# Kernel tuning notes

Hardware: AMD Instinct MI355X
Metric: run time of the kernel (lower is better)

## Reference

```python
import jax, jax.numpy as jnp
import numpy as np

EPS = 1e-5


def conv2d(x, w, b, groups=1):
    # x: NCHW, w: OIHW, stride 1, SAME padding (== padding=k//2 for odd k)
    y = jax.lax.conv_general_dilated(
        x, w, window_strides=(1, 1), padding='SAME',
        dimension_numbers=('NCHW', 'OIHW', 'NCHW'),
        feature_group_count=groups)
    return y + b[None, :, None, None]


def gelu(x):
    return jax.nn.gelu(x, approximate=False)  # torch default GELU is exact erf


def adaptive_feature_norm(x, gamma, beta, s1w, s1b, s2w, s2b):
    # stats_net: GAP -> 1x1 conv -> ReLU -> 1x1 conv -> chunk into (gamma_a, beta_a)
    pooled = x.mean(axis=(2, 3), keepdims=True)                 # [B,C,1,1]
    h = jax.nn.relu(conv2d(pooled, s1w, s1b))
    stats = conv2d(h, s2w, s2b)                                 # [B,2C,1,1]
    ag, ab = jnp.split(stats, 2, axis=1)
    mean = x.mean(axis=(2, 3), keepdims=True)
    n = x.shape[2] * x.shape[3]
    var = ((x - mean) ** 2).sum(axis=(2, 3), keepdims=True) / (n - 1)  # unbiased, torch.var_mean default
    x_norm = (x - mean) * jax.lax.rsqrt(var + EPS)
    return (1 + ag) * gamma * x_norm + ab * beta


def setup_inputs() -> dict:
    key = jax.random.key(0)
    ks = jax.random.split(key, 40)
    B, C, H, W = 16, 256, 96, 96
    c4 = C // 4

    def n(k, shape, s=0.02):
        return jax.random.normal(k, shape, dtype=jnp.float32) * s

    inp = dict(
        x=jax.random.normal(ks[0], (B, C, H, W), dtype=jnp.float32),
        # branch1 conv1: dim -> dim//4, 3x3
        b1_conv1_w=n(ks[1], (c4, C, 3, 3)), b1_conv1_b=jnp.zeros((c4,), jnp.float32),
        # AFN on dim//4
        afn1_gamma=jnp.ones((1, c4, 1, 1), jnp.float32), afn1_beta=jnp.zeros((1, c4, 1, 1), jnp.float32),
        afn1_s1_w=n(ks[2], (c4 // 4, c4, 1, 1)), afn1_s1_b=jnp.zeros((c4 // 4,), jnp.float32),
        afn1_s2_w=n(ks[3], (c4 * 2, c4 // 4, 1, 1)), afn1_s2_b=jnp.zeros((c4 * 2,), jnp.float32),
        # branch1 conv2: dim//4 -> dim, 3x3
        b1_conv2_w=n(ks[4], (C, c4, 3, 3)), b1_conv2_b=jnp.zeros((C,), jnp.float32),
        # AFN on dim
        afn2_gamma=jnp.ones((1, C, 1, 1), jnp.float32), afn2_beta=jnp.zeros((1, C, 1, 1), jnp.float32),
        afn2_s1_w=n(ks[5], (c4, C, 1, 1)), afn2_s1_b=jnp.zeros((c4,), jnp.float32),
        afn2_s2_w=n(ks[6], (C * 2, c4, 1, 1)), afn2_s2_b=jnp.zeros((C * 2,), jnp.float32),
        # attention qkv/proj (1x1 convs)
        qkv_w=n(ks[7], (3 * C, C, 1, 1)), qkv_b=jnp.zeros((3 * C,), jnp.float32),
        proj_w=n(ks[8], (C, C, 1, 1)), proj_b=jnp.zeros((C,), jnp.float32),
        # 3 frequency decomposition branches, stacked
        # grouped 3x3 conv: groups=C//4, in=C (4 per group), out=C//4 (1 per group) -> weight [C//4, 4, 3, 3]
        fd_dw_w=n(ks[9], (3, c4, 4, 3, 3)), fd_dw_b=jnp.zeros((3, c4), jnp.float32),
        fd_pw_w=n(ks[10], (3, C, c4, 1, 1)), fd_pw_b=jnp.zeros((3, C), jnp.float32),
        freq_weights=jnp.ones((3,), jnp.float32),
        # router: GAP -> 1x1 conv -> softmax over 2 routes
        router_w=n(ks[11], (2, C, 1, 1)), router_b=jnp.zeros((2,), jnp.float32),
    )
    return inp


def reference(x,
              b1_conv1_w, b1_conv1_b, afn1_gamma, afn1_beta, afn1_s1_w, afn1_s1_b, afn1_s2_w, afn1_s2_b,
              b1_conv2_w, b1_conv2_b, afn2_gamma, afn2_beta, afn2_s1_w, afn2_s1_b, afn2_s2_w, afn2_s2_b,
              qkv_w, qkv_b, proj_w, proj_b, fd_dw_w, fd_dw_b, fd_pw_w, fd_pw_b, freq_weights,
              router_w, router_b):
    B, C, H, W = x.shape
    num_heads = 8
    hd = C // num_heads
    scale = C ** (-0.5)

    # ---- router ----
    pooled = x.mean(axis=(2, 3), keepdims=True)
    route = jax.nn.softmax(conv2d(pooled, router_w, router_b), axis=1)  # [B,2,1,1]

    # ---- branch1: conv -> AFN -> GELU -> conv -> AFN ----
    h = conv2d(x, b1_conv1_w, b1_conv1_b)
    h = adaptive_feature_norm(h, afn1_gamma, afn1_beta, afn1_s1_w, afn1_s1_b, afn1_s2_w, afn1_s2_b)
    h = gelu(h)
    h = conv2d(h, b1_conv2_w, b1_conv2_b)
    out1 = adaptive_feature_norm(h, afn2_gamma, afn2_beta, afn2_s1_w, afn2_s1_b, afn2_s2_w, afn2_s2_b)

    # ---- branch2: multi-scale frequency attention ----
    qkv = conv2d(x, qkv_w, qkv_b).reshape(B, 3, num_heads, hd, H, W)
    q, k, v = qkv[:, 0], qkv[:, 1], qkv[:, 2]          # [B, nh, hd, H, W]
    # attn over spatial rows: q @ k^T contracts W -> [B, nh, hd, H, H]
    attn = jnp.einsum('bndhw,bndgw->bndhg', q, k) * scale
    attn = jax.nn.softmax(attn, axis=-1)
    a = jnp.einsum('bndhg,bndgw->bndhw', attn, v)       # [B, nh, hd, H, W]
    # torch: .transpose(1, 2).reshape(B, C, H, W)  (hd-major channel order)
    a = a.transpose(0, 2, 1, 3, 4).reshape(B, C, H, W)
    x_attn = conv2d(a, proj_w, proj_b)

    fw = jax.nn.softmax(freq_weights, axis=0)
    freq_out = 0.0
    for i in range(3):
        f = conv2d(x, fd_dw_w[i], fd_dw_b[i], groups=C // 4)
        f = conv2d(gelu(f), fd_pw_w[i], fd_pw_b[i])
        freq_out = freq_out + fw[i] * f
    out2 = x_attn + freq_out

    return x + route[:, 0:1, :, :] * out1 + route[:, 1:2, :, :] * out2
```

## Files before the change

### kernel.cpp

```cpp
#include <hip/hip_runtime.h>
#include <hip/hip_bf16.h>
#include <math.h>
#include <stdint.h>

#define BB 16
#define CC 256
#define C4 64
#define HH 96
#define WW 96
#define HW 9216
#define EPSF 1e-5f

using bf16x8 = __attribute__((ext_vector_type(8))) short;
using bf16x4 = __attribute__((ext_vector_type(4))) short;
using f32x4  = __attribute__((ext_vector_type(4))) float;

#define GLD16(g, l) \
    __builtin_amdgcn_global_load_lds((const __attribute__((address_space(1))) unsigned int*)(g), \
                                     (__attribute__((address_space(3))) unsigned int*)(l), 16, 0, 0)

__device__ inline float bf2f_bits(short s) {
    return __uint_as_float(((unsigned int)(unsigned short)s) << 16);
}
__device__ inline short f2bf_bits(float f) {
    unsigned int u = __float_as_uint(f);
    return (short)((u + 0x7fffu + ((u >> 16) & 1u)) >> 16);
}

__global__ void zero_kernel(unsigned int* __restrict__ p) { p[threadIdx.x] = 0u; }

__global__ void channel_stats_kernel(const float* __restrict__ x,
                                     float* __restrict__ mean_out,
                                     float* __restrict__ istd_out) {
    int bc = blockIdx.x;
    const float* p = x + (size_t)bc * HW;
    float s = 0.f, ss = 0.f;
    for (int i = threadIdx.x; i < HW; i += 256) { float v = p[i]; s += v; ss += v * v; }
    __shared__ float red[256], red2[256];
    red[threadIdx.x] = s; red2[threadIdx.x] = ss;
    __syncthreads();
    for (int off = 128; off > 0; off >>= 1) {
        if (threadIdx.x < off) { red[threadIdx.x] += red[threadIdx.x + off]; red2[threadIdx.x] += red2[threadIdx.x + off]; }
        __syncthreads();
    }
    if (threadIdx.x == 0) {
        float sum = red[0], sumsq = red2[0];
        float m = sum / (float)HW;
        float var = (sumsq - sum * m) / (float)(HW - 1);
        mean_out[bc] = m;
        istd_out[bc] = rsqrtf(var + EPSF);
    }
}

__global__ void router_kernel(const float* __restrict__ pooled, const float* __restrict__ rw,
                              const float* __restrict__ rb, const float* __restrict__ fwts,
                              float* __restrict__ route, float* __restrict__ fw) {
    int t = threadIdx.x;
    if (t < BB) {
        float l0 = rb[0], l1 = rb[1];
        for (int c = 0; c < CC; ++c) {
            float p = pooled[t * CC + c];
            l0 += p * rw[c];
            l1 += p * rw[CC + c];
        }
        float m = fmaxf(l0, l1);
        float e0 = __expf(l0 - m), e1 = __expf(l1 - m);
        float inv = 1.f / (e0 + e1);
        route[t * 2 + 0] = e0 * inv;
        route[t * 2 + 1] = e1 * inv;
    }
    if (t == BB) {
        float a = fwts[0], b = fwts[1], c = fwts[2];
        float m = fmaxf(a, fmaxf(b, c));
        float e0 = __expf(a - m), e1 = __expf(b - m), e2 = __expf(c - m);
        float inv = 1.f / (e0 + e1 + e2);
        fw[0] = e0 * inv; fw[1] = e1 * inv; fw[2] = e2 * inv;
    }
}

__global__ void pack_w3x3_kernel(const float* __restrict__ w, __hip_bfloat16* __restrict__ wt,
                                 int COUT, int CINW) {
    int idx = blockIdx.x * 256 + threadIdx.x;
    int total = COUT * 9 * CINW;
    if (idx >= total) return;
    int ci = idx % CINW; int rest = idx / CINW; int tau = rest % 9; int co = rest / 9;
    wt[idx] = __float2bfloat16(w[((size_t)co * CINW + ci) * 9 + tau]);
}

__global__ void cast_w_kernel(const float* __restrict__ w, __hip_bfloat16* __restrict__ o, int n) {
    int idx = blockIdx.x * 256 + threadIdx.x;
    if (idx < n) o[idx] = __float2bfloat16(w[idx]);
}

__global__ void fuse_freq_w_kernel(const float* __restrict__ pww, const float* __restrict__ pwb,
                                   const float* __restrict__ fw, __hip_bfloat16* __restrict__ wtf,
                                   float* __restrict__ fbias) {
    int co = blockIdx.x; int t = threadIdx.x;
    int i = t >> 6, g = t & 63;
    wtf[co * 192 + t] = __float2bfloat16(fw[i] * pww[((size_t)(i * 256 + co)) * 64 + g]);
    if (t == 0) fbias[co] = fw[0] * pwb[co] + fw[1] * pwb[256 + co] + fw[2] * pwb[512 + co];
}

__device__ inline float to_f32(float v) { return v; }
__device__ inline float to_f32(__hip_bfloat16 v) { return __bfloat162float(v); }

template <typename TIN, int CIN>
__global__ __launch_bounds__(256) void transpose_pm_kernel(const TIN* __restrict__ x,
                                                           __hip_bfloat16* __restrict__ xt) {
    __shared__ float s[32][33];
    int p0 = blockIdx.x * 32, c0 = blockIdx.y * 32, b = blockIdx.z;
    int tx = threadIdx.x, ty = threadIdx.y;
    const TIN* xp = x + ((size_t)b * CIN + c0) * HW + p0;
#pragma unroll
    for (int i = 0; i < 4; ++i) {
        int c = ty * 4 + i;
        s[c][tx] = to_f32(xp[(size_t)c * HW + tx]);
    }
    __syncthreads();
    __hip_bfloat16* yp = xt + ((size_t)b * HW + p0) * CIN + c0;
#pragma unroll
    for (int i = 0; i < 4; ++i) {
        int r = ty * 4 + i;
        yp[(size_t)r * CIN + tx] = __float2bfloat16(s[tx][r]);
    }
}

template <int BM, int BN, int TSH, int KC, int CDIM, int EPI, int CO_TOT>
__global__ __launch_bounds__(256) void mfma_gemm_kernel(const short* __restrict__ A,
                                                        const short* __restrict__ Bx,
                                                        const short* __restrict__ zp,
                                                        const float* __restrict__ bias,
                                                        const float* __restrict__ route,
                                                        void* __restrict__ Y,
                                                        int bin0, int bout0) {
    constexpr int WM = BM / 2, WN = BN / 2;
    constexpr int FM = WM / 16, FN = WN / 16;
    constexpr int KB = KC / 32;
    constexpr int NA = BM / 16;
    constexpr int NB = BN / 16;
    __shared__ __align__(16) short As[BM * 32];
    __shared__ __align__(16) short Bs[BN * 32];
    int tid = threadIdx.x;
    int wid = tid >> 6, lane = tid & 63;
    int wy = wid >> 1, wx = wid & 1;
    int lane16 = lane & 15, quad = lane >> 4;
    int lrow = lane >> 2, lchk = lane & 3;
    int co0 = blockIdx.x * BM;
    int n0 = blockIdx.y * BN;
    int bin = blockIdx.z + bin0;
    int bout = blockIdx.z + bout0;

    f32x4 acc[FM][FN];
#pragma unroll
    for (int i = 0; i < FM; ++i)
#pragma unroll
        for (int j = 0; j < FN; ++j) acc[i][j] = (f32x4){0.f, 0.f, 0.f, 0.f};

    const short* Bbase = Bx + (size_t)bin * HW * CDIM;

    for (int tau = 0; tau < TSH; ++tau) {
        int dh = tau / 3, dw = tau % 3;
        int off = (TSH > 1) ? (dh - 1) * 96 + (dw - 1) : 0;
        for (int kb = 0; kb < KB; ++kb) {
            int kc0 = kb * 32;
#pragma unroll
            for (int t = 0; t < NA / 4; ++t) {
                int inst = wid * (NA / 4) + t;
                int row = inst * 16 + lrow;
                const short* g = A + (size_t)(co0 + row) * (TSH * KC) + tau * KC + kc0 + lchk * 8;
                GLD16(g, &As[inst * 512]);
            }
#pragma unroll
            for (int t = 0; t < NB / 4; ++t) {
                int inst = wid * (NB / 4) + t;
                int row = inst * 16 + lrow;
                int n = n0 + row;
                const short* g;
                if (TSH > 1) {
                    int h = n / 96, w = n - h * 96;
                    int hh = h + dh - 1, ww2 = w + dw - 1;
                    bool valid = ((unsigned)hh < 96u) && ((unsigned)ww2 < 96u);
                    g = valid ? (Bbase + (size_t)(n + off) * CDIM + kc0 + lchk * 8) : zp;
                } else {
                    g = Bbase + (size_t)n * CDIM + kc0 + lchk * 8;
                }
                GLD16(g, &Bs[inst * 512]);
            }
            __syncthreads();
            bf16x8 af[FM], bfr[FN];
#pragma unroll
            for (int i = 0; i < FM; ++i)
                af[i] = *(const bf16x8*)&As[(wy * WM + i * 16 + lane16) * 32 + quad * 8];
#pragma unroll
            for (int j = 0; j < FN; ++j)
                bfr[j] = *(const bf16x8*)&Bs[(wx * WN + j * 16 + lane16) * 32 + quad * 8];
#pragma unroll
            for (int i = 0; i < FM; ++i)
#pragma unroll
                for (int j = 0; j < FN; ++j)
                    acc[i][j] = __builtin_amdgcn_mfma_f32_16x16x32_bf16(af[i], bfr[j], acc[i][j], 0, 0, 0);
            __syncthreads();
        }
    }
    float scale = 1.f;
    if (EPI == 2) scale = route[bin * 2 + 1];
#pragma unroll
    for (int i = 0; i < FM; ++i) {
        int co_l = co0 + wy * WM + i * 16 + quad * 4;
#pragma unroll
        for (int j = 0; j < FN; ++j) {
            int pix = n0 + wx * WN + j * 16 + lane16;
#pragma unroll
            for (int r = 0; r < 4; ++r) {
                int co = co_l + r;
                float v = acc[i][j][r] + bias[co];
                size_t idx = ((size_t)(bout * CO_TOT + co)) * HW + pix;
                if (EPI == 0) ((float*)Y)[idx] = v;
                else if (EPI == 1) ((__hip_bfloat16*)Y)[idx] = __float2bfloat16(v);
                else ((float*)Y)[idx] += scale * v;
            }
        }
    }
}

template <int CH, int HID>
__global__ void afn_mlp_kernel(const float* __restrict__ mean,
                               const float* __restrict__ s1w, const float* __restrict__ s1b,
                               const float* __restrict__ s2w, const float* __restrict__ s2b,
                               float* __restrict__ ag, float* __restrict__ ab) {
    int b = blockIdx.x;
    __shared__ float hbuf[HID];
    int t = threadIdx.x;
    if (t < HID) {
        float s = s1b[t];
        for (int c = 0; c < CH; ++c) s += mean[b * CH + c] * s1w[t * CH + c];
        hbuf[t] = fmaxf(s, 0.f);
    }
    __syncthreads();
    if (t < 2 * CH) {
        float s = s2b[t];
#pragma unroll
        for (int k = 0; k < HID; ++k) s += hbuf[k] * s2w[t * HID + k];
        if (t < CH) ag[b * CH + t] = s;
        else        ab[b * CH + (t - CH)] = s;
    }
}

template <int CH, bool GELU>
__global__ void afn_apply_kernel(float* __restrict__ hbuf_g, const float* __restrict__ mean,
                                 const float* __restrict__ istd, const float* __restrict__ ag,
                                 const float* __restrict__ ab, const float* __restrict__ gamma,
                                 const float* __restrict__ beta) {
    int p = blockIdx.x * 256 + threadIdx.x;
    int c = blockIdx.y, b = blockIdx.z;
    int bc = b * CH + c;
    float scale = (1.f + ag[bc]) * gamma[c] * istd[bc];
    float shift = ab[bc] * beta[c];
    float m = mean[bc];
    float* ptr = hbuf_g + (size_t)bc * HW + p;
    float v = (*ptr - m) * scale + shift;
    if (GELU) v = 0.5f * v * (1.f + erff(v * 0.70710678118654752f));
    *ptr = v;
}

__global__ void combine_kernel(const float* __restrict__ x, const float* __restrict__ out1,
                               const float* __restrict__ route, float* __restrict__ out) {
    int b = blockIdx.y;
    size_t i = (size_t)b * CC * HW + (size_t)blockIdx.x * 256 + threadIdx.x;
    float r0 = route[b * 2];
    out[i] = x[i] + r0 * out1[i];
}

__global__ __launch_bounds__(256) void vtrans_kernel(const __hip_bfloat16* __restrict__ qkv,
                                                     __hip_bfloat16* __restrict__ vt) {
    __shared__ __hip_bfloat16 s[32][34];
    int th = blockIdx.x / 3, tw = blockIdx.x % 3;
    int c = blockIdx.y, b = blockIdx.z;
    int tx = threadIdx.x, ty = threadIdx.y;
    const __hip_bfloat16* ip = qkv + ((size_t)b * 768 + 512 + c) * HW + (size_t)(th * 32) * 96 + tw * 32;
#pragma unroll
    for (int i = 0; i < 4; ++i) s[ty * 4 + i][tx] = ip[(size_t)(ty * 4 + i) * 96 + tx];
    __syncthreads();
    __hip_bfloat16* op = vt + ((size_t)b * 256 + c) * HW + (size_t)(tw * 32) * 96 + th * 32;
#pragma unroll
    for (int i = 0; i < 4; ++i) op[(size_t)(ty * 4 + i) * 96 + tx] = s[tx][ty * 4 + i];
}

__global__ __launch_bounds__(256) void attn_mfma_kernel(const __hip_bfloat16* __restrict__ qkv,
                                                        const __hip_bfloat16* __restrict__ vt,
                                                        __hip_bfloat16* __restrict__ a, int bout0) {
    int d = blockIdx.x, n = blockIdx.y, b = blockIdx.z;
    __shared__ __align__(16) __hip_bfloat16 Ps[96 * 104];
    int t = threadIdx.x;
    int lane = t & 63, wid = t >> 6;
    int wy = wid >> 1, wx = wid & 1;
    int lane16 = lane & 15, quad = lane >> 4;

    const __hip_bfloat16* qp = qkv + ((size_t)b * 768 + n * 32 + d) * HW;
    const __hip_bfloat16* kp = qp + (size_t)256 * HW;
    const __hip_bfloat16* vp = vt + ((size_t)b * 256 + n * 32 + d) * HW;

    f32x4 acc[3][3];
#pragma unroll
    for (int i = 0; i < 3; ++i)
#pragma unroll
        for (int j = 0; j < 3; ++j) acc[i][j] = (f32x4){0.f, 0.f, 0.f, 0.f};

#pragma unroll
    for (int kb = 0; kb < 3; ++kb) {
        int kc = kb * 32 + quad * 8;
        bf16x8 af[3], bfr[3];
#pragma unroll
        for (int i = 0; i < 3; ++i)
            af[i] = *(const bf16x8*)(qp + (size_t)(wy * 48 + i * 16 + lane16) * 96 + kc);
#pragma unroll
        for (int j = 0; j < 3; ++j)
            bfr[j] = *(const bf16x8*)(kp + (size_t)(wx * 48 + j * 16 + lane16) * 96 + kc);
#pragma unroll
        for (int i = 0; i < 3; ++i)
#pragma unroll
            for (int j = 0; j < 3; ++j)
                acc[i][j] = __builtin_amdgcn_mfma_f32_16x16x32_bf16(af[i], bfr[j], acc[i][j], 0, 0, 0);
    }

    const float scale = 0.0625f;
#pragma unroll
    for (int i = 0; i < 3; ++i) {
        int rbase = wy * 48 + i * 16 + quad * 4;
#pragma unroll
        for (int j = 0; j < 3; ++j) {
            int col = wx * 48 + j * 16 + lane16;
#pragma unroll
            for (int r = 0; r < 4; ++r)
                Ps[(rbase + r) * 104 + col] = __float2bfloat16(acc[i][j][r] * scale);
        }
    }
    __syncthreads();

    if (t < 192) {
        int row = t >> 1, hh = t & 1;
        const bf16x4* pr4 = (const bf16x4*)&Ps[row * 104 + hh * 48];
        float vb[48];
        float m = -1e30f;
#pragma unroll
        for (int j4 = 0; j4 < 12; ++j4) {
            bf16x4 u = pr4[j4];
#pragma unroll
            for (int e = 0; e < 4; ++e) {
                float f = bf2f_bits(u[e]);
                vb[j4 * 4 + e] = f;
                m = fmaxf(m, f);
            }
        }
        m = fmaxf(m, __shfl_xor(m, 1));
        float ssum = 0.f;
#pragma unroll
        for (int j2 = 0; j2 < 48; ++j2) { vb[j2] = __expf(vb[j2] - m); ssum += vb[j2]; }
        ssum += __shfl_xor(ssum, 1);
        float inv = 1.f / ssum;
        bf16x4* pw4 = (bf16x4*)&Ps[row * 104 + hh * 48];
#pragma unroll
        for (int j4 = 0; j4 < 12; ++j4) {
            bf16x4 o;
#pragma unroll
            for (int e = 0; e < 4; ++e) o[e] = f2bf_bits(vb[j4 * 4 + e] * inv);
            pw4[j4] = o;
        }
    }
    __syncthreads();

#pragma unroll
    for (int i = 0; i < 3; ++i)
#pragma unroll
        for (int j = 0; j < 3; ++j) acc[i][j] = (f32x4){0.f, 0.f, 0.f, 0.f};

#pragma unroll
    for (int kb = 0; kb < 3; ++kb) {
        int kc = kb * 32 + quad * 8;
        bf16x8 af[3], bfr[3];
#pragma unroll
        for (int i = 0; i < 3; ++i)
            af[i] = *(const bf16x8*)&Ps[(wy * 48 + i * 16 + lane16) * 104 + kc];
#pragma unroll
        for (int j = 0; j < 3; ++j)
            bfr[j] = *(const bf16x8*)(vp + (size_t)(wx * 48 + j * 16 + lane16) * 96 + kc);
#pragma unroll
        for (int i = 0; i < 3; ++i)
#pragma unroll
            for (int j = 0; j < 3; ++j)
                acc[i][j] = __builtin_amdgcn_mfma_f32_16x16x32_bf16(af[i], bfr[j], acc[i][j], 0, 0, 0);
    }

    __hip_bfloat16* ap = a + ((size_t)(bout0 + b) * CC + (d * 8 + n)) * HW;
#pragma unroll
    for (int i = 0; i < 3; ++i) {
        int rbase = wy * 48 + i * 16 + quad * 4;
#pragma unroll
        for (int j = 0; j < 3; ++j) {
            int col = wx * 48 + j * 16 + lane16;
#pragma unroll
            for (int r = 0; r < 4; ++r)
                ap[(size_t)(rbase + r) * 96 + col] = __float2bfloat16(acc[i][j][r]);
        }
    }
}

__global__ __launch_bounds__(256) void freqdw_kernel(const float* __restrict__ x,
                                                     const float* __restrict__ wgt,
                                                     const float* __restrict__ bias,
                                                     __hip_bfloat16* __restrict__ f, int cbase) {
    int p = blockIdx.x * 256 + threadIdx.x;
    int g = blockIdx.y;
    int b = blockIdx.z;
    int h = p / WW, w = p % WW;
    float acc = bias[g];
    const float* wq = wgt + g * 36;
#pragma unroll
    for (int q = 0; q < 4; ++q) {
        const float* xc = x + ((size_t)b * CC + 4 * g + q) * HW;
#pragma unroll
        for (int dh = 0; dh < 3; ++dh) {
            int hh = h + dh - 1;
            bool hv = (hh >= 0) && (hh < HH);
#pragma unroll
            for (int dw = 0; dw < 3; ++dw) {
                int ww2 = w + dw - 1;
                bool v = hv && (ww2 >= 0) && (ww2 < WW);
                float xv = v ? xc[hh * WW + ww2] : 0.f;
                acc += xv * wq[q * 9 + dh * 3 + dw];
            }
        }
    }
    acc = 0.5f * acc * (1.f + erff(acc * 0.70710678118654752f));
    f[((size_t)b * 192 + cbase + g) * HW + p] = __float2bfloat16(acc);
}

extern "C" void kernel_launch(void* const* d_in, const int* in_sizes, int n_in,
                              void* d_out, int out_size, void* d_ws, size_t ws_size,
                              hipStream_t stream) {
    const float* x    = (const float*)d_in[0];
    const float* c1w  = (const float*)d_in[1];
    const float* c1b  = (const float*)d_in[2];
    const float* g1   = (const float*)d_in[3];
    const float* be1  = (const float*)d_in[4];
    const float* s1w1 = (const float*)d_in[5];
    const float* s1b1 = (const float*)d_in[6];
    const float* s2w1 = (const float*)d_in[7];
    const float* s2b1 = (const float*)d_in[8];
    const float* c2w  = (const float*)d_in[9];
    const float* c2b  = (const float*)d_in[10];
    const float* g2   = (const float*)d_in[11];
    const float* be2  = (const float*)d_in[12];
    const float* s1w2 = (const float*)d_in[13];
    const float* s1b2 = (const float*)d_in[14];
    const float* s2w2 = (const float*)d_in[15];
    const float* s2b2 = (const float*)d_in[16];
    const float* qkvw = (const float*)d_in[17];
    const float* qkvb = (const float*)d_in[18];
    const float* pjw  = (const float*)d_in[19];
    const float* pjb  = (const float*)d_in[20];
    const float* dww  = (const float*)d_in[21];
    const float* dwb  = (const float*)d_in[22];
    const float* pww  = (const float*)d_in[23];
    const float* pwb  = (const float*)d_in[24];
    const float* fwts = (const float*)d_in[25];
    const float* rw   = (const float*)d_in[26];
    const float* rb   = (const float*)d_in[27];
    float* out = (float*)d_out;
    (void)ws_size;

    char* ws = (char*)d_ws;
    float* h2 = (float*)ws;
    __hip_bfloat16* qkvs = (__hip_bfloat16*)ws;
    __hip_bfloat16* at_t = (__hip_bfloat16*)ws;
    __hip_bfloat16* fall = (__hip_bfloat16*)ws;
    __hip_bfloat16* f_t  = (__hip_bfloat16*)(ws + 56623104ULL);
    __hip_bfloat16* vt = (__hip_bfloat16*)(ws + 113246208ULL);
    float* h1 = (float*)(ws + 150994944ULL);
    __hip_bfloat16* h1t = (__hip_bfloat16*)(ws + 188743680ULL);
    __hip_bfloat16* xt = (__hip_bfloat16*)(ws + 207618048ULL);
    __hip_bfloat16* at = xt;
    const size_t TB = 283115520ULL;
    short* zp = (short*)(ws + TB);
    float* stats = (float*)(ws + TB + 256);
    float* pooled_x = stats;
    float* route    = pooled_x + 4096;
    float* fw       = route + 32;
    float* mean1    = fw + 4;
    float* istd1    = mean1 + 1024;
    float* ag1      = istd1 + 1024;
    float* ab1      = ag1 + 1024;
    float* mean2    = ab1 + 1024;
    float* istd2    = mean2 + 4096;
    float* ag2      = istd2 + 4096;
    float* ab2      = ag2 + 4096;
    float* fbias    = ab2 + 4096;
    float* dummy    = fbias + 256;
    char* wbase = (char*)(dummy + 4096);
    __hip_bfloat16* wt1  = (__hip_bfloat16*)wbase;
    __hip_bfloat16* wt2  = (__hip_bfloat16*)(wbase + 294912);
    __hip_bfloat16* qw16 = (__hip_bfloat16*)(wbase + 589824);
    __hip_bfloat16* pw16 = (__hip_bfloat16*)(wbase + 983040);
    __hip_bfloat16* wtf  = (__hip_bfloat16*)(wbase + 1114112);

    zero_kernel<<<1, 64, 0, stream>>>((unsigned int*)zp);

    channel_stats_kernel<<<dim3(BB * CC), 256, 0, stream>>>(x, pooled_x, dummy);
    router_kernel<<<1, 64, 0, stream>>>(pooled_x, rw, rb, fwts, route, fw);

    pack_w3x3_kernel<<<576, 256, 0, stream>>>(c1w, wt1, 64, 256);
    pack_w3x3_kernel<<<576, 256, 0, stream>>>(c2w, wt2, 256, 64);
    cast_w_kernel<<<768, 256, 0, stream>>>(qkvw, qw16, 768 * 256);
    cast_w_kernel<<<256, 256, 0, stream>>>(pjw, pw16, 256 * 256);
    fuse_freq_w_kernel<<<256, 192, 0, stream>>>(pww, pwb, fw, wtf, fbias);

    transpose_pm_kernel<float, 256><<<dim3(288, 8, 16), dim3(32, 8), 0, stream>>>(x, xt);

    mfma_gemm_kernel<64, 128, 9, 256, 256, 0, 64>
        <<<dim3(1, 72, 16), 256, 0, stream>>>((const short*)wt1, (const short*)xt, zp, c1b, nullptr, h1, 0, 0);
    channel_stats_kernel<<<dim3(BB * C4), 256, 0, stream>>>(h1, mean1, istd1);
    afn_mlp_kernel<64, 16><<<dim3(BB), 128, 0, stream>>>(mean1, s1w1, s1b1, s2w1, s2b1, ag1, ab1);
    afn_apply_kernel<64, true><<<dim3(36, 64, 16), 256, 0, stream>>>(h1, mean1, istd1, ag1, ab1, g1, be1);
    transpose_pm_kernel<float, 64><<<dim3(288, 2, 16), dim3(32, 8), 0, stream>>>(h1, h1t);
    mfma_gemm_kernel<128, 128, 9, 64, 64, 0, 256>
        <<<dim3(2, 72, 16), 256, 0, stream>>>((const short*)wt2, (const short*)h1t, zp, c2b, nullptr, h2, 0, 0);
    channel_stats_kernel<<<dim3(BB * CC), 256, 0, stream>>>(h2, mean2, istd2);
    afn_mlp_kernel<256, 64><<<dim3(BB), 512, 0, stream>>>(mean2, s1w2, s1b2, s2w2, s2b2, ag2, ab2);
    afn_apply_kernel<256, false><<<dim3(36, 256, 16), 256, 0, stream>>>(h2, mean2, istd2, ag2, ab2, g2, be2);

    combine_kernel<<<dim3(9216, 16), 256, 0, stream>>>(x, h2, route, out);

    for (int half = 0; half < 2; ++half) {
        mfma_gemm_kernel<128, 128, 1, 256, 256, 1, 768>
            <<<dim3(6, 72, 8), 256, 0, stream>>>((const short*)qw16, (const short*)xt, zp, qkvb,
                                                 nullptr, qkvs, half * 8, 0);
        vtrans_kernel<<<dim3(9, 256, 8), dim3(32, 8), 0, stream>>>(qkvs, vt);
        attn_mfma_kernel<<<dim3(32, 8, 8), 256, 0, stream>>>(qkvs, vt, at, half * 8);
    }
    transpose_pm_kernel<__hip_bfloat16, 256><<<dim3(288, 8, 16), dim3(32, 8), 0, stream>>>(at, at_t);
    mfma_gemm_kernel<128, 128, 1, 256, 256, 2, 256>
        <<<dim3(2, 72, 16), 256, 0, stream>>>((const short*)pw16, (const short*)at_t, zp, pjb, route, out, 0, 0);

    for (int i = 0; i < 3; ++i)
        freqdw_kernel<<<dim3(36, 64, 16), 256, 0, stream>>>(x, dww + i * C4 * 36, dwb + i * C4, fall, i * 64);
    transpose_pm_kernel<__hip_bfloat16, 192><<<dim3(288, 6, 16), dim3(32, 8), 0, stream>>>(fall, f_t);
    mfma_gemm_kernel<128, 128, 1, 192, 192, 2, 256>
        <<<dim3(2, 72, 16), 256, 0, stream>>>((const short*)wtf, (const short*)f_t, zp, fbias, route, out, 0, 0);
}
```

Measured before the change: 1.481 ms.

## Fuse channel stats into GEMM epilogues, merge proj and freq GEMMs, fuse AFN combine

Drops the separate channel_stats passes. Pooling of x is computed in the transpose kernel with atomics, and per-channel sum and sum-of-squares for the two conv outputs are accumulated in the GEMM epilogue. The AFN2 apply and final combine become one vectorized kernel. The projection GEMM and the frequency pointwise GEMM are concatenated into a single K=448 GEMM with merged bias, and the three depthwise convs run in one kernel that reads x once. The aim is fewer full-tensor memory passes and launches, at the cost of atomic contention and slightly different float summation order.

```diff
diff --git a/kernel.cpp b/kernel.cpp
--- a/kernel.cpp
+++ b/kernel.cpp
@@ -27,39 +27,20 @@
     return (short)((u + 0x7fffu + ((u >> 16) & 1u)) >> 16);
 }
 
-__global__ void zero_kernel(unsigned int* __restrict__ p) { p[threadIdx.x] = 0u; }
-
-__global__ void channel_stats_kernel(const float* __restrict__ x,
-                                     float* __restrict__ mean_out,
-                                     float* __restrict__ istd_out) {
-    int bc = blockIdx.x;
-    const float* p = x + (size_t)bc * HW;
-    float s = 0.f, ss = 0.f;
-    for (int i = threadIdx.x; i < HW; i += 256) { float v = p[i]; s += v; ss += v * v; }
-    __shared__ float red[256], red2[256];
-    red[threadIdx.x] = s; red2[threadIdx.x] = ss;
-    __syncthreads();
-    for (int off = 128; off > 0; off >>= 1) {
-        if (threadIdx.x < off) { red[threadIdx.x] += red[threadIdx.x + off]; red2[threadIdx.x] += red2[threadIdx.x + off]; }
-        __syncthreads();
-    }
-    if (threadIdx.x == 0) {
-        float sum = red[0], sumsq = red2[0];
-        float m = sum / (float)HW;
-        float var = (sumsq - sum * m) / (float)(HW - 1);
-        mean_out[bc] = m;
-        istd_out[bc] = rsqrtf(var + EPSF);
-    }
+__global__ void zero_n_kernel(unsigned int* __restrict__ p, int n) {
+    int i = blockIdx.x * 256 + threadIdx.x;
+    if (i < n) p[i] = 0u;
 }
 
 __global__ void router_kernel(const float* __restrict__ pooled, const float* __restrict__ rw,
                               const float* __restrict__ rb, const float* __restrict__ fwts,
                               float* __restrict__ route, float* __restrict__ fw) {
     int t = threadIdx.x;
+    const float invhw = 1.f / (float)HW;
     if (t < BB) {
         float l0 = rb[0], l1 = rb[1];
         for (int c = 0; c < CC; ++c) {
-            float p = pooled[t * CC + c];
+            float p = pooled[t * CC + c] * invhw;
             l0 += p * rw[c];
             l1 += p * rw[CC + c];
         }
@@ -92,22 +73,30 @@
     if (idx < n) o[idx] = __float2bfloat16(w[idx]);
 }
 
-__global__ void fuse_freq_w_kernel(const float* __restrict__ pww, const float* __restrict__ pwb,
-                                   const float* __restrict__ fw, __hip_bfloat16* __restrict__ wtf,
-                                   float* __restrict__ fbias) {
+__global__ void cast_w448_kernel(const float* __restrict__ w, __hip_bfloat16* __restrict__ A448) {
+    int idx = blockIdx.x * 256 + threadIdx.x;
+    int co = idx >> 8, ci = idx & 255;
+    A448[co * 448 + ci] = __float2bfloat16(w[idx]);
+}
+
+__global__ void fuse_freq_w448_kernel(const float* __restrict__ pww, const float* __restrict__ pwb,
+                                      const float* __restrict__ pjb, const float* __restrict__ fw,
+                                      __hip_bfloat16* __restrict__ A448, float* __restrict__ fb448) {
     int co = blockIdx.x; int t = threadIdx.x;
     int i = t >> 6, g = t & 63;
-    wtf[co * 192 + t] = __float2bfloat16(fw[i] * pww[((size_t)(i * 256 + co)) * 64 + g]);
-    if (t == 0) fbias[co] = fw[0] * pwb[co] + fw[1] * pwb[256 + co] + fw[2] * pwb[512 + co];
+    A448[co * 448 + 256 + t] = __float2bfloat16(fw[i] * pww[((size_t)(i * 256 + co)) * 64 + g]);
+    if (t == 0) fb448[co] = pjb[co] + fw[0] * pwb[co] + fw[1] * pwb[256 + co] + fw[2] * pwb[512 + co];
 }
 
 __device__ inline float to_f32(float v) { return v; }
 __device__ inline float to_f32(__hip_bfloat16 v) { return __bfloat162float(v); }
 
-template <typename TIN, int CIN>
+template <typename TIN, int CIN, int OSTR, bool POOL>
 __global__ __launch_bounds__(256) void transpose_pm_kernel(const TIN* __restrict__ x,
-                                                           __hip_bfloat16* __restrict__ xt) {
+                                                           __hip_bfloat16* __restrict__ xt,
+                                                           float* __restrict__ pooled) {
     __shared__ float s[32][33];
+    __shared__ float ps[8][32];
     int p0 = blockIdx.x * 32, c0 = blockIdx.y * 32, b = blockIdx.z;
     int tx = threadIdx.x, ty = threadIdx.y;
     const TIN* xp = x + ((size_t)b * CIN + c0) * HW + p0;
@@ -117,21 +106,36 @@
         s[c][tx] = to_f32(xp[(size_t)c * HW + tx]);
     }
     __syncthreads();
-    __hip_bfloat16* yp = xt + ((size_t)b * HW + p0) * CIN + c0;
+    __hip_bfloat16* yp = xt + ((size_t)b * HW + p0) * OSTR + c0;
 #pragma unroll
     for (int i = 0; i < 4; ++i) {
         int r = ty * 4 + i;
-        yp[(size_t)r * CIN + tx] = __float2bfloat16(s[tx][r]);
-    }
-}
-
-template <int BM, int BN, int TSH, int KC, int CDIM, int EPI, int CO_TOT>
+        yp[(size_t)r * OSTR + tx] = __float2bfloat16(s[tx][r]);
+    }
+    if (POOL) {
+        float l4 = 0.f;
+#pragma unroll
+        for (int i = 0; i < 4; ++i) l4 += s[tx][ty * 4 + i];
+        ps[ty][tx] = l4;
+        __syncthreads();
+        if (ty == 0) {
+            float tot = 0.f;
+#pragma unroll
+            for (int k = 0; k < 8; ++k) tot += ps[k][tx];
+            atomicAdd(&pooled[b * CIN + c0 + tx], tot);
+        }
+    }
+}
+
+template <int BM, int BN, int TSH, int KC, int CDIM, int EPI, int CO_TOT, bool STATS>
 __global__ __launch_bounds__(256) void mfma_gemm_kernel(const short* __restrict__ A,
                                                         const short* __restrict__ Bx,
                                                         const short* __restrict__ zp,
                                                         const float* __restrict__ bias,
                                                         const float* __restrict__ route,
                                                         void* __restrict__ Y,
+                                                        float* __restrict__ ssum,
+                                                        float* __restrict__ sssq,
                                                         int bin0, int bout0) {
     constexpr int WM = BM / 2, WN = BN / 2;
     constexpr int FM = WM / 16, FN = WN / 16;
@@ -204,6 +208,13 @@
     }
     float scale = 1.f;
     if (EPI == 2) scale = route[bin * 2 + 1];
+    float sl[FM][4], ql[FM][4];
+    if (STATS) {
+#pragma unroll
+        for (int i = 0; i < FM; ++i)
+#pragma unroll
+            for (int r = 0; r < 4; ++r) { sl[i][r] = 0.f; ql[i][r] = 0.f; }
+    }
 #pragma unroll
     for (int i = 0; i < FM; ++i) {
         int co_l = co0 + wy * WM + i * 16 + quad * 4;
@@ -218,9 +229,39 @@
                 if (EPI == 0) ((float*)Y)[idx] = v;
                 else if (EPI == 1) ((__hip_bfloat16*)Y)[idx] = __float2bfloat16(v);
                 else ((float*)Y)[idx] += scale * v;
+                if (STATS) { sl[i][r] += v; ql[i][r] += v * v; }
             }
         }
     }
+    if (STATS) {
+#pragma unroll
+        for (int i = 0; i < FM; ++i) {
+            int co_l = co0 + wy * WM + i * 16 + quad * 4;
+#pragma unroll
+            for (int r = 0; r < 4; ++r) {
+                float s = sl[i][r], q = ql[i][r];
+                s += __shfl_xor(s, 1); q += __shfl_xor(q, 1);
+                s += __shfl_xor(s, 2); q += __shfl_xor(q, 2);
+                s += __shfl_xor(s, 4); q += __shfl_xor(q, 4);
+                s += __shfl_xor(s, 8); q += __shfl_xor(q, 8);
+                if (lane16 == 0) {
+                    int bc = bout * CO_TOT + co_l + r;
+                    atomicAdd(&ssum[bc], s);
+                    atomicAdd(&sssq[bc], q);
+                }
+            }
+        }
+    }
+}
+
+__global__ void afn_finalize_kernel(const float* __restrict__ s, const float* __restrict__ q,
+                                    float* __restrict__ mean, float* __restrict__ istd, int n) {
+    int i = blockIdx.x * 256 + threadIdx.x;
+    if (i >= n) return;
+    float m = s[i] / (float)HW;
+    float var = (q[i] - s[i] * m) / (float)(HW - 1);
+    mean[i] = m;
+    istd[i] = rsqrtf(var + EPSF);
 }
 
 template <int CH, int HID>
@@ -263,12 +304,30 @@
     *ptr = v;
 }
 
-__global__ void combine_kernel(const float* __restrict__ x, const float* __restrict__ out1,
-                               const float* __restrict__ route, float* __restrict__ out) {
-    int b = blockIdx.y;
-    size_t i = (size_t)b * CC * HW + (size_t)blockIdx.x * 256 + threadIdx.x;
+__global__ __launch_bounds__(256) void afn_combine_kernel(const float* __restrict__ x,
+                                                          const float* __restrict__ h2,
+                                                          const float* __restrict__ mean,
+                                                          const float* __restrict__ istd,
+                                                          const float* __restrict__ ag,
+                                                          const float* __restrict__ ab,
+                                                          const float* __restrict__ gamma,
+                                                          const float* __restrict__ beta,
+                                                          const float* __restrict__ route,
+                                                          float* __restrict__ out) {
+    int p4 = blockIdx.x * 256 + threadIdx.x;
+    int c = blockIdx.y, b = blockIdx.z;
+    int bc = b * CC + c;
+    float scale = (1.f + ag[bc]) * gamma[c] * istd[bc];
+    float shift = ab[bc] * beta[c];
+    float m = mean[bc];
     float r0 = route[b * 2];
-    out[i] = x[i] + r0 * out1[i];
+    size_t base = (size_t)bc * (HW / 4) + p4;
+    const f32x4 xv = ((const f32x4*)x)[base];
+    const f32x4 hv = ((const f32x4*)h2)[base];
+    f32x4 o;
+#pragma unroll
+    for (int e = 0; e < 4; ++e) o[e] = xv[e] + r0 * ((hv[e] - m) * scale + shift);
+    ((f32x4*)out)[base] = o;
 }
 
 __global__ __launch_bounds__(256) void vtrans_kernel(const __hip_bfloat16* __restrict__ qkv,
@@ -405,16 +464,18 @@
     }
 }
 
-__global__ __launch_bounds__(256) void freqdw_kernel(const float* __restrict__ x,
-                                                     const float* __restrict__ wgt,
-                                                     const float* __restrict__ bias,
-                                                     __hip_bfloat16* __restrict__ f, int cbase) {
+__global__ __launch_bounds__(256) void freq3_kernel(const float* __restrict__ x,
+                                                    const float* __restrict__ dww,
+                                                    const float* __restrict__ dwb,
+                                                    __hip_bfloat16* __restrict__ f) {
     int p = blockIdx.x * 256 + threadIdx.x;
     int g = blockIdx.y;
     int b = blockIdx.z;
     int h = p / WW, w = p % WW;
-    float acc = bias[g];
-    const float* wq = wgt + g * 36;
+    float a0 = dwb[g], a1 = dwb[64 + g], a2 = dwb[128 + g];
+    const float* w0 = dww + g * 36;
+    const float* w1 = dww + (64 + g) * 36;
+    const float* w2 = dww + (128 + g) * 36;
 #pragma unroll
     for (int q = 0; q < 4; ++q) {
         const float* xc = x + ((size_t)b * CC + 4 * g + q) * HW;
@@ -427,12 +488,20 @@
                 int ww2 = w + dw - 1;
                 bool v = hv && (ww2 >= 0) && (ww2 < WW);
                 float xv = v ? xc[hh * WW + ww2] : 0.f;
-                acc += xv * wq[q * 9 + dh * 3 + dw];
+                int wi = q * 9 + dh * 3 + dw;
+                a0 += xv * w0[wi];
+                a1 += xv * w1[wi];
+                a2 += xv * w2[wi];
             }
         }
     }
-    acc = 0.5f * acc * (1.f + erff(acc * 0.70710678118654752f));
-    f[((size_t)b * 192 + cbase + g) * HW + p] = __float2bfloat16(acc);
+    a0 = 0.5f * a0 * (1.f + erff(a0 * 0.70710678118654752f));
+    a1 = 0.5f * a1 * (1.f + erff(a1 * 0.70710678118654752f));
+    a2 = 0.5f * a2 * (1.f + erff(a2 * 0.70710678118654752f));
+    size_t base = ((size_t)b * 192 + g) * HW + p;
+    f[base] = __float2bfloat16(a0);
+    f[base + (size_t)64 * HW] = __float2bfloat16(a1);
+    f[base + (size_t)128 * HW] = __float2bfloat16(a2);
 }
 
 extern "C" void kernel_launch(void* const* d_in, const int* in_sizes, int n_in,
@@ -472,9 +541,8 @@
     char* ws = (char*)d_ws;
     float* h2 = (float*)ws;
     __hip_bfloat16* qkvs = (__hip_bfloat16*)ws;
-    __hip_bfloat16* at_t = (__hip_bfloat16*)ws;
     __hip_bfloat16* fall = (__hip_bfloat16*)ws;
-    __hip_bfloat16* f_t  = (__hip_bfloat16*)(ws + 56623104ULL);
+    __hip_bfloat16* ftA = (__hip_bfloat16*)(ws + 56623104ULL);
     __hip_bfloat16* vt = (__hip_bfloat16*)(ws + 113246208ULL);
     float* h1 = (float*)(ws + 150994944ULL);
     __hip_bfloat16* h1t = (__hip_bfloat16*)(ws + 188743680ULL);
@@ -482,68 +550,73 @@
     __hip_bfloat16* at = xt;
     const size_t TB = 283115520ULL;
     short* zp = (short*)(ws + TB);
-    float* stats = (float*)(ws + TB + 256);
-    float* pooled_x = stats;
-    float* route    = pooled_x + 4096;
-    float* fw       = route + 32;
-    float* mean1    = fw + 4;
-    float* istd1    = mean1 + 1024;
-    float* ag1      = istd1 + 1024;
-    float* ab1      = ag1 + 1024;
-    float* mean2    = ab1 + 1024;
-    float* istd2    = mean2 + 4096;
-    float* ag2      = istd2 + 4096;
-    float* ab2      = ag2 + 4096;
-    float* fbias    = ab2 + 4096;
-    float* dummy    = fbias + 256;
-    char* wbase = (char*)(dummy + 4096);
+    float* zf = (float*)(ws + TB + 256);
+    float* ssum1  = zf;
+    float* sssq1  = zf + 1024;
+    float* ssum2  = zf + 2048;
+    float* sssq2  = zf + 6144;
+    float* pooled = zf + 10240;
+    float* route  = zf + 14336;
+    float* fw     = zf + 14368;
+    float* mean1  = zf + 14372;
+    float* istd1  = zf + 15396;
+    float* ag1    = zf + 16420;
+    float* ab1    = zf + 17444;
+    float* mean2  = zf + 18468;
+    float* istd2  = zf + 22564;
+    float* ag2    = zf + 26660;
+    float* ab2    = zf + 30756;
+    float* fb448  = zf + 34852;
+    char* wbase = (char*)(zf + 35108);
     __hip_bfloat16* wt1  = (__hip_bfloat16*)wbase;
     __hip_bfloat16* wt2  = (__hip_bfloat16*)(wbase + 294912);
     __hip_bfloat16* qw16 = (__hip_bfloat16*)(wbase + 589824);
-    __hip_bfloat16* pw16 = (__hip_bfloat16*)(wbase + 983040);
-    __hip_bfloat16* wtf  = (__hip_bfloat16*)(wbase + 1114112);
-
-    zero_kernel<<<1, 64, 0, stream>>>((unsigned int*)zp);
-
-    channel_stats_kernel<<<dim3(BB * CC), 256, 0, stream>>>(x, pooled_x, dummy);
-    router_kernel<<<1, 64, 0, stream>>>(pooled_x, rw, rb, fwts, route, fw);
+    __hip_bfloat16* A448 = (__hip_bfloat16*)(wbase + 983040);
+
+    zero_n_kernel<<<57, 256, 0, stream>>>((unsigned int*)zp, 14400);
+
+    transpose_pm_kernel<float, 256, 256, true>
+        <<<dim3(288, 8, 16), dim3(32, 8), 0, stream>>>(x, xt, pooled);
+    router_kernel<<<1, 64, 0, stream>>>(pooled, rw, rb, fwts, route, fw);
 
     pack_w3x3_kernel<<<576, 256, 0, stream>>>(c1w, wt1, 64, 256);
     pack_w3x3_kernel<<<576, 256, 0, stream>>>(c2w, wt2, 256, 64);
     cast_w_kernel<<<768, 256, 0, stream>>>(qkvw, qw16, 768 * 256);
-    cast_w_kernel<<<256, 256, 0, stream>>>(pjw, pw16, 256 * 256);
-    fuse_freq_w_kernel<<<256, 192, 0, stream>>>(pww, pwb, fw, wtf, fbias);
-
-    transpose_pm_kernel<float, 256><<<dim3(288, 8, 16), dim3(32, 8), 0, stream>>>(x, xt);
-
-    mfma_gemm_kernel<64, 128, 9, 256, 256, 0, 64>
-        <<<dim3(1, 72, 16), 256, 0, stream>>>((const short*)wt1, (const short*)xt, zp, c1b, nullptr, h1, 0, 0);
-    channel_stats_kernel<<<dim3(BB * C4), 256, 0, stream>>>(h1, mean1, istd1);
+    cast_w448_kernel<<<256, 256, 0, stream>>>(pjw, A448);
+    fuse_freq_w448_kernel<<<256, 192, 0, stream>>>(pww, pwb, pjb, fw, A448, fb448);
+
+    mfma_gemm_kernel<64, 128, 9, 256, 256, 0, 64, true>
+        <<<dim3(1, 72, 16), 256, 0, stream>>>((const short*)wt1, (const short*)xt, zp, c1b,
+                                              nullptr, h1, ssum1, sssq1, 0, 0);
+    afn_finalize_kernel<<<4, 256, 0, stream>>>(ssum1, sssq1, mean1, istd1, BB * C4);
     afn_mlp_kernel<64, 16><<<dim3(BB), 128, 0, stream>>>(mean1, s1w1, s1b1, s2w1, s2b1, ag1, ab1);
     afn_apply_kernel<64, true><<<dim3(36, 64, 16), 256, 0, stream>>>(h1, mean1, istd1, ag1, ab1, g1, be1);
-    transpose_pm_kernel<float, 64><<<dim3(288, 2, 16), dim3(32, 8), 0, stream>>>(h1, h1t);
-    mfma_gemm_kernel<128, 128, 9, 64, 64, 0, 256>
-        <<<dim3(2, 72, 16), 256, 0, stream>>>((const short*)wt2, (const short*)h1t, zp, c2b, nullptr, h2, 0, 0);
-    channel_stats_kernel<<<dim3(BB * CC), 256, 0, stream>>>(h2, mean2, istd2);
+    transpose_pm_kernel<float, 64, 64, false>
+        <<<dim3(288, 2, 16), dim3(32, 8), 0, stream>>>(h1, h1t, nullptr);
+    mfma_gemm_kernel<128, 128, 9, 64, 64, 0, 256, true>
+        <<<dim3(2, 72, 16), 256, 0, stream>>>((const short*)wt2, (const short*)h1t, zp, c2b,
+                                              nullptr, h2, ssum2, sssq2, 0, 0);
+    afn_finalize_kernel<<<16, 256, 0, stream>>>(ssum2, sssq2, mean2, istd2, BB * CC);
     afn_mlp_kernel<256, 64><<<dim3(BB), 512, 0, stream>>>(mean2, s1w2, s1b2, s2w2, s2b2, ag2, ab2);
-    afn_apply_kernel<256, false><<<dim3(36, 256, 16), 256, 0, stream>>>(h2, mean2, istd2, ag2, ab2, g2, be2);
-
-    combine_kernel<<<dim3(9216, 16), 256, 0, stream>>>(x, h2, route, out);
+    afn_combine_kernel<<<dim3(9, 256, 16), 256, 0, stream>>>(x, h2, mean2, istd2, ag2, ab2,
+                                                             g2, be2, route, out);
 
     for (int half = 0; half < 2; ++half) {
-        mfma_gemm_kernel<128, 128, 1, 256, 256, 1, 768>
+        mfma_gemm_kernel<128, 128, 1, 256, 256, 1, 768, false>
             <<<dim3(6, 72, 8), 256, 0, stream>>>((const short*)qw16, (const short*)xt, zp, qkvb,
-                                                 nullptr, qkvs, half * 8, 0);
+                                                 nullptr, qkvs, nullptr, nullptr, half * 8, 0);
         vtrans_kernel<<<dim3(9, 256, 8), dim3(32, 8), 0, stream>>>(qkvs, vt);
         attn_mfma_kernel<<<dim3(32, 8, 8), 256, 0, stream>>>(qkvs, vt, at, half * 8);
     }
-    transpose_pm_kernel<__hip_bfloat16, 256><<<dim3(288, 8, 16), dim3(32, 8), 0, stream>>>(at, at_t);
-    mfma_gemm_kernel<128, 128, 1, 256, 256, 2, 256>
-        <<<dim3(2, 72, 16), 256, 0, stream>>>((const short*)pw16, (const short*)at_t, zp, pjb, route, out, 0, 0);
-
-    for (int i = 0; i < 3; ++i)
-        freqdw_kernel<<<dim3(36, 64, 16), 256, 0, stream>>>(x, dww + i * C4 * 36, dwb + i * C4, fall, i * 64);
-    transpose_pm_kernel<__hip_bfloat16, 192><<<dim3(288, 6, 16), dim3(32, 8), 0, stream>>>(fall, f_t);
-    mfma_gemm_kernel<128, 128, 1, 192, 192, 2, 256>
-        <<<dim3(2, 72, 16), 256, 0, stream>>>((const short*)wtf, (const short*)f_t, zp, fbias, route, out, 0, 0);
-}
+
+    freq3_kernel<<<dim3(36, 64, 16), 256, 0, stream>>>(x, dww, dwb, fall);
+
+    transpose_pm_kernel<__hip_bfloat16, 256, 448, false>
+        <<<dim3(288, 8, 16), dim3(32, 8), 0, stream>>>(at, ftA, nullptr);
+    transpose_pm_kernel<__hip_bfloat16, 192, 448, false>
+        <<<dim3(288, 6, 16), dim3(32, 8), 0, stream>>>(fall, ftA + 256, nullptr);
+
+    mfma_gemm_kernel<128, 128, 1, 448, 448, 2, 256, false>
+        <<<dim3(2, 72, 16), 256, 0, stream>>>((const short*)A448, (const short*)ftA, zp, fb448,
+                                              route, out, nullptr, nullptr, 0, 0);
+}
```

New measurement: 1.224 ms. 17.3% less time.
